# Kernel tuning notes

Measured on AMD Instinct MI355X. Metric: run time of the kernel, lower is better.

The kernel has to match this reference:

```python
import jax, jax.numpy as jnp
import numpy as np

SCALE = 32 ** (-0.5)  # hardcoded in the original module, independent of head_size

def setup_inputs() -> dict:
    key = jax.random.key(0)
    k1, k2, k3, k4 = jax.random.split(key, 4)
    B, T, E, H = 8, 4096, 2048, 128
    x = jax.random.normal(k1, (B, T, E), dtype=jnp.float32)
    Wq = jax.random.normal(k2, (E, H), dtype=jnp.float32) * (E ** -0.5)
    Wk = jax.random.normal(k3, (E, H), dtype=jnp.float32) * (E ** -0.5)
    Wv = jax.random.normal(k4, (E, H), dtype=jnp.float32) * (E ** -0.5)
    return {"x": x, "Wq": Wq, "Wk": Wk, "Wv": Wv}

def reference(x, Wq, Wk, Wv):
    # q,k,v: [B,T,H]
    q = jnp.einsum('bte,eh->bth', x, Wq)
    k = jnp.einsum('bte,eh->bth', x, Wk)
    v = jnp.einsum('bte,eh->bth', x, Wv)
    # wei: [B, T(query), T(key)]
    wei = jnp.einsum('bqh,bkh->bqk', q, k) * SCALE
    # NOTE: original uses F.softmax(wei, dim=1) -> normalize over the QUERY axis
    wei = jax.nn.softmax(wei, axis=1)
    # dropout prob is 0 in this deterministic baseline (eval mode)
    out = jnp.einsum('bqk,bkh->bqh', wei, v)
    return out
```

## Files before the change

### kernel.cpp

```cpp
#include <hip/hip_runtime.h>
#include <hip/hip_bf16.h>
#include <hip/hip_fp16.h>

#define Bn 8
#define Tn 4096
#define En 2048
#define Hn 128

typedef __attribute__((ext_vector_type(8))) short bf16x8;
typedef __attribute__((ext_vector_type(4))) float f32x4;
typedef __attribute__((ext_vector_type(4))) unsigned int u32x4;

typedef const __attribute__((address_space(1))) unsigned int* gptr_t;
typedef __attribute__((address_space(3))) unsigned int* lptr_t;

static __device__ __forceinline__ void gload16(const void* g, void* l) {
    __builtin_amdgcn_global_load_lds((gptr_t)g, (lptr_t)l, 16, 0, 0);
}

static __device__ __forceinline__ unsigned short f2bf(float f) {
    union { float f; unsigned u; } v; v.f = f;
    unsigned r = v.u + 0x7FFFu + ((v.u >> 16) & 1u);
    return (unsigned short)(r >> 16);
}
static __device__ __forceinline__ unsigned cvtpk(float lo, float hi) {
    unsigned r;
    asm volatile("v_cvt_pk_bf16_f32 %0, %1, %2" : "=v"(r) : "v"(lo), "v"(hi));
    return r;
}

#define MFMA16(a, b, c) __builtin_amdgcn_mfma_f32_16x16x32_bf16((a), (b), (c), 0, 0, 0)
#define EXP2F(x) __builtin_amdgcn_exp2f(x)
#define WAIT_VM_PUB(N) do { asm volatile("s_waitcnt vmcnt(" #N ")" ::: "memory"); \
                            __builtin_amdgcn_sched_barrier(0); \
                            __builtin_amdgcn_s_barrier(); \
                            __builtin_amdgcn_sched_barrier(0); } while (0)
#define LGKM_BARRIER() do { asm volatile("s_waitcnt lgkmcnt(0)" ::: "memory"); \
                            __builtin_amdgcn_s_barrier(); \
                            __builtin_amdgcn_sched_barrier(0); } while (0)

__global__ __launch_bounds__(256) void prep_w(const float* __restrict__ Wq,
                                              const float* __restrict__ Wk,
                                              const float* __restrict__ Wv,
                                              unsigned short* __restrict__ Wt) {
    int idx = blockIdx.x * 256 + threadIdx.x;
    int w = idx / (En * Hn);
    int rem = idx - w * (En * Hn);
    int kx = rem >> 7;
    int n  = rem & 127;
    const float* W = (w == 0) ? Wq : (w == 1) ? Wk : Wv;
    float f = W[rem];
    if (w == 0) f *= (0.17677669529663687f * 1.4426950408889634f);
    Wt[(size_t)w * En * Hn + (size_t)n * En + kx] = f2bf(f);
}

__global__ __launch_bounds__(256, 3) void qkv_mfma(const float* __restrict__ x,
                                                   const unsigned short* __restrict__ Wt,
                                                   unsigned short* __restrict__ qs,
                                                   unsigned short* __restrict__ ks,
                                                   unsigned short* __restrict__ vT) {
    __shared__ __align__(16) float Al[128][64];
    __shared__ __align__(16) unsigned short Bl[128][64];
    const int bid = blockIdx.x;
    const int w = bid % 3;
    const int m0 = (bid / 3) * 128;
    const int b = m0 >> 12;
    const int tb = m0 & (Tn - 1);
    const int t = threadIdx.x;
    const int lane = t & 63, wid = t >> 6;
    const int wr = (wid >> 1) * 64, wc = (wid & 1) * 64;
    const int fr = lane & 15, fq = lane >> 4;
    const unsigned short* Wb = Wt + (size_t)w * En * Hn;
    const int aR = lane >> 4, aC = lane & 15;
    const int bR = lane >> 3, bC = lane & 7;

    f32x4 acc[4][4] = {};
    for (int k0 = 0; k0 < En; k0 += 64) {
        __syncthreads();
        #pragma unroll
        for (int s = 0; s < 8; ++s) {
            int seg = wid * 8 + s;
            int r = seg * 4 + aR;
            gload16(&x[(size_t)(m0 + r) * En + k0 + ((aC ^ (r & 15)) * 4)],
                    (char*)Al + seg * 1024 + lane * 16);
        }
        #pragma unroll
        for (int s = 0; s < 4; ++s) {
            int seg = wid * 4 + s;
            int r = seg * 8 + bR;
            gload16(&Wb[(size_t)r * En + k0 + ((bC ^ (r & 7)) * 8)],
                    (char*)Bl + seg * 1024 + lane * 16);
        }
        __syncthreads();
        #pragma unroll
        for (int ksub = 0; ksub < 2; ++ksub) {
            bf16x8 av[4], bv[4];
            #pragma unroll
            for (int mi = 0; mi < 4; ++mi) {
                int row = wr + mi * 16 + fr;
                const char* base = (const char*)Al + row * 256;
                int c0 = ksub * 8 + fq * 2;
                f32x4 a0 = *(const f32x4*)(base + ((c0 ^ (row & 15)) << 4));
                f32x4 a1 = *(const f32x4*)(base + (((c0 + 1) ^ (row & 15)) << 4));
                u32x4 pk;
                pk[0] = cvtpk(a0[0], a0[1]);
                pk[1] = cvtpk(a0[2], a0[3]);
                pk[2] = cvtpk(a1[0], a1[1]);
                pk[3] = cvtpk(a1[2], a1[3]);
                av[mi] = *reinterpret_cast<bf16x8*>(&pk);
            }
            #pragma unroll
            for (int ni = 0; ni < 4; ++ni) {
                int row = wc + ni * 16 + fr;
                int ch = (ksub * 4 + fq) ^ (row & 7);
                bv[ni] = *reinterpret_cast<const bf16x8*>((const char*)Bl + row * 128 + ch * 16);
            }
            #pragma unroll
            for (int mi = 0; mi < 4; ++mi)
                #pragma unroll
                for (int ni = 0; ni < 4; ++ni)
                    acc[mi][ni] = MFMA16(av[mi], bv[ni], acc[mi][ni]);
        }
    }

    if (w < 2) {
        unsigned short* out = (w == 0) ? qs : ks;
        #pragma unroll
        for (int mi = 0; mi < 4; ++mi)
            #pragma unroll
            for (int ni = 0; ni < 4; ++ni)
                #pragma unroll
                for (int r = 0; r < 4; ++r) {
                    int row = m0 + wr + mi * 16 + fq * 4 + r;
                    int col = wc + ni * 16 + fr;
                    out[(size_t)row * Hn + col] = f2bf(acc[mi][ni][r]);
                }
    } else {
        #pragma unroll
        for (int mi = 0; mi < 4; ++mi)
            #pragma unroll
            for (int ni = 0; ni < 4; ++ni)
                #pragma unroll
                for (int r = 0; r < 4; ++r) {
                    int tt = tb + wr + mi * 16 + fq * 4 + r;
                    int h  = wc + ni * 16 + fr;
                    vT[((size_t)b * Hn + h) * Tn + tt] = f2bf(acc[mi][ni][r]);
                }
    }
}

__global__ __launch_bounds__(256, 3) void stats_qk(const unsigned short* __restrict__ qs,
                                                   const unsigned short* __restrict__ ks,
                                                   float2* __restrict__ part) {
    __shared__ __align__(16) char smem[49152];
    const int bid = blockIdx.x;
    const int b = bid & 7;
    const int rest = bid >> 3;
    const int kt = rest & 63;
    const int qh = rest >> 6;
    const int k0 = kt * 64;
    const unsigned short* qb = qs + (size_t)b * Tn * Hn;
    const unsigned short* kb = ks + (size_t)b * Tn * Hn;
    const int t = threadIdx.x;
    const int lane = t & 63, wid = t >> 6;
    const int wk = wid >> 1, wq = wid & 1;
    const int fr = lane & 15, fq = lane >> 4;
    const int srow = t >> 4, schk = t & 15;

    #pragma unroll
    for (int it = 0; it < 4; ++it) {
        int r = it * 16 + srow;
        gload16(&kb[(size_t)(k0 + r) * Hn + ((schk ^ (r & 15)) * 8)],
                smem + it * 4096 + t * 16);
        gload16(&qb[(size_t)(qh * 2048 + r) * Hn + ((schk ^ (r & 15)) * 8)],
                smem + 16384 + it * 4096 + t * 16);
    }
    __syncthreads();
    bf16x8 av[2][4];
    #pragma unroll
    for (int mi = 0; mi < 2; ++mi)
        #pragma unroll
        for (int kc = 0; kc < 4; ++kc) {
            int row = wk * 32 + mi * 16 + fr;
            int ch = (kc * 4 + fq) ^ (row & 15);
            av[mi][kc] = *reinterpret_cast<const bf16x8*>(smem + row * 256 + ch * 16);
        }

    float m[2][4], l[2][4];
    #pragma unroll
    for (int mi = 0; mi < 2; ++mi)
        #pragma unroll
        for (int r = 0; r < 4; ++r) { m[mi][r] = -INFINITY; l[mi][r] = 0.f; }

    for (int step = 0; step < 32; ++step) {
        const int cur = step & 1;
        const int qn = qh * 2048 + ((step + 1) & 31) * 64;
        #pragma unroll
        for (int it = 0; it < 4; ++it) {
            int r = it * 16 + srow;
            gload16(&qb[(size_t)(qn + r) * Hn + ((schk ^ (r & 15)) * 8)],
                    smem + 16384 + (cur ^ 1) * 16384 + it * 4096 + t * 16);
        }
        WAIT_VM_PUB(4);
        const char* Qc = smem + 16384 + cur * 16384;
        f32x4 acc[2][2] = {};
        __builtin_amdgcn_s_setprio(1);
        #pragma unroll
        for (int kc = 0; kc < 4; ++kc) {
            bf16x8 bv[2];
            #pragma unroll
            for (int ni = 0; ni < 2; ++ni) {
                int row = wq * 32 + ni * 16 + fr;
                int ch = (kc * 4 + fq) ^ (row & 15);
                bv[ni] = *reinterpret_cast<const bf16x8*>(Qc + row * 256 + ch * 16);
            }
            #pragma unroll
            for (int mi = 0; mi < 2; ++mi)
                #pragma unroll
                for (int ni = 0; ni < 2; ++ni)
                    acc[mi][ni] = MFMA16(av[mi][kc], bv[ni], acc[mi][ni]);
        }
        __builtin_amdgcn_s_setprio(0);
        #pragma unroll
        for (int mi = 0; mi < 2; ++mi)
            #pragma unroll
            for (int r = 0; r < 4; ++r) {
                float v0 = acc[mi][0][r], v1 = acc[mi][1][r];
                float mn = fmaxf(m[mi][r], fmaxf(v0, v1));
                l[mi][r] = l[mi][r] * EXP2F(m[mi][r] - mn) + EXP2F(v0 - mn) + EXP2F(v1 - mn);
                m[mi][r] = mn;
            }
        LGKM_BARRIER();
    }
    #pragma unroll
    for (int off = 1; off <= 8; off <<= 1) {
        #pragma unroll
        for (int mi = 0; mi < 2; ++mi)
            #pragma unroll
            for (int r = 0; r < 4; ++r) {
                float mo = __shfl_xor(m[mi][r], off);
                float lo = __shfl_xor(l[mi][r], off);
                float mn = fmaxf(m[mi][r], mo);
                l[mi][r] = l[mi][r] * EXP2F(m[mi][r] - mn) + lo * EXP2F(mo - mn);
                m[mi][r] = mn;
            }
    }
    if (fr == 0) {
        #pragma unroll
        for (int mi = 0; mi < 2; ++mi)
            #pragma unroll
            for (int r = 0; r < 4; ++r) {
                int k = k0 + wk * 32 + mi * 16 + fq * 4 + r;
                part[((size_t)b * Tn + k) * 4 + qh * 2 + wq] = make_float2(m[mi][r], l[mi][r]);
            }
    }
}

__global__ __launch_bounds__(256) void stats_comb(const float2* __restrict__ part,
                                                  float* __restrict__ mr) {
    int g = blockIdx.x * 256 + threadIdx.x;
    const float2* pp = part + (size_t)g * 4;
    float2 p0 = pp[0], p1 = pp[1], p2 = pp[2], p3 = pp[3];
    float M = fmaxf(fmaxf(p0.x, p1.x), fmaxf(p2.x, p3.x));
    float L = p0.y * EXP2F(p0.x - M) + p1.y * EXP2F(p1.x - M) +
              p2.y * EXP2F(p2.x - M) + p3.y * EXP2F(p3.x - M);
    mr[g] = M + __log2f(L);
}

__global__ __launch_bounds__(256, 2) void attn_pv(const unsigned short* __restrict__ qs,
                                                  const unsigned short* __restrict__ ks,
                                                  const unsigned short* __restrict__ vT,
                                                  const float* __restrict__ mr,
                                                  float* __restrict__ out) {
    __shared__ __align__(16) char smem[73728];
    char* Pb = smem + 65536;
    const int bid = blockIdx.x;
    const int b = bid & 7;
    const int q0 = (bid >> 3) * 64;
    const unsigned short* qg = qs + (size_t)b * Tn * Hn;
    const unsigned short* kg = ks + (size_t)b * Tn * Hn;
    const unsigned short* vg = vT + (size_t)b * Hn * Tn;
    const float* mrb = mr + (size_t)b * Tn;
    const int t = threadIdx.x;
    const int lane = t & 63, wid = t >> 6;
    const int wk = wid >> 1, wq = wid & 1;
    const int fr = lane & 15, fq = lane >> 4;
    const int srow16 = t >> 4, schk16 = t & 15;
    const int srow8 = t >> 3, schk8 = t & 7;

    bf16x8 bq[2][4];
    #pragma unroll
    for (int ni = 0; ni < 2; ++ni)
        #pragma unroll
        for (int kc = 0; kc < 4; ++kc) {
            int row = q0 + wq * 32 + ni * 16 + fr;
            bq[ni][kc] = *reinterpret_cast<const bf16x8*>(&qg[(size_t)row * Hn + kc * 32 + fq * 8]);
        }
    #pragma unroll
    for (int it = 0; it < 4; ++it) {
        int r = it * 16 + srow16;
        gload16(&kg[(size_t)r * Hn + ((schk16 ^ (r & 15)) * 8)], smem + it * 4096 + t * 16);
        int rv = it * 32 + srow8;
        gload16(&vg[(size_t)rv * Tn + ((schk8 ^ (rv & 7)) * 8)],
                smem + 32768 + it * 4096 + t * 16);
    }
    __syncthreads();

    f32x4 acc_o[4][2] = {};
    for (int kt = 0; kt < 64; ++kt) {
        const int cur = kt & 1;
        const int k0 = kt * 64;
        float4 mk0 = *reinterpret_cast<const float4*>(&mrb[k0 + wk * 32 + fq * 4]);
        float4 mk1 = *reinterpret_cast<const float4*>(&mrb[k0 + wk * 32 + 16 + fq * 4]);
        __builtin_amdgcn_sched_barrier(0);
        {
            const int knr = ((kt + 1) & 63) * 64;
            #pragma unroll
            for (int it = 0; it < 4; ++it) {
                int r = it * 16 + srow16;
                gload16(&kg[(size_t)(knr + r) * Hn + ((schk16 ^ (r & 15)) * 8)],
                        smem + (cur ^ 1) * 16384 + it * 4096 + t * 16);
                int rv = it * 32 + srow8;
                gload16(&vg[(size_t)rv * Tn + knr + ((schk8 ^ (rv & 7)) * 8)],
                        smem + 32768 + (cur ^ 1) * 16384 + it * 4096 + t * 16);
            }
        }
        WAIT_VM_PUB(8);
        const char* Kc = smem + cur * 16384;
        f32x4 acc_s[2][2] = {};
        __builtin_amdgcn_s_setprio(1);
        #pragma unroll
        for (int kc = 0; kc < 4; ++kc) {
            bf16x8 avk[2];
            #pragma unroll
            for (int mi = 0; mi < 2; ++mi) {
                int row = wk * 32 + mi * 16 + fr;
                int ch = (kc * 4 + fq) ^ (row & 15);
                avk[mi] = *reinterpret_cast<const bf16x8*>(Kc + row * 256 + ch * 16);
            }
            #pragma unroll
            for (int mi = 0; mi < 2; ++mi)
                #pragma unroll
                for (int ni = 0; ni < 2; ++ni)
                    acc_s[mi][ni] = MFMA16(avk[mi], bq[ni][kc], acc_s[mi][ni]);
        }
        __builtin_amdgcn_s_setprio(0);
        #pragma unroll
        for (int mi = 0; mi < 2; ++mi) {
            float4 mk = mi ? mk1 : mk0;
            #pragma unroll
            for (int ni = 0; ni < 2; ++ni) {
                float e0 = EXP2F(acc_s[mi][ni][0] - mk.x);
                float e1 = EXP2F(acc_s[mi][ni][1] - mk.y);
                float e2 = EXP2F(acc_s[mi][ni][2] - mk.z);
                float e3 = EXP2F(acc_s[mi][ni][3] - mk.w);
                int q = wq * 32 + ni * 16 + fr;
                int chunk = (wk * 4 + mi * 2 + (fq >> 1)) ^ (q & 7);
                *reinterpret_cast<uint2*>(Pb + q * 128 + chunk * 16 + (fq & 1) * 8) =
                    make_uint2(cvtpk(e0, e1), cvtpk(e2, e3));
            }
        }
        LGKM_BARRIER();
        const char* Vc = smem + 32768 + cur * 16384;
        __builtin_amdgcn_s_setprio(1);
        #pragma unroll
        for (int kc = 0; kc < 2; ++kc) {
            bf16x8 bp[2];
            #pragma unroll
            for (int ni = 0; ni < 2; ++ni) {
                int qrow = wq * 32 + ni * 16 + fr;
                int ch = (kc * 4 + fq) ^ (qrow & 7);
                bp[ni] = *reinterpret_cast<const bf16x8*>(Pb + qrow * 128 + ch * 16);
            }
            #pragma unroll
            for (int mi = 0; mi < 4; ++mi) {
                int row = wk * 64 + mi * 16 + fr;
                int ch = (kc * 4 + fq) ^ (row & 7);
                bf16x8 avv = *reinterpret_cast<const bf16x8*>(Vc + row * 128 + ch * 16);
                #pragma unroll
                for (int ni = 0; ni < 2; ++ni)
                    acc_o[mi][ni] = MFMA16(avv, bp[ni], acc_o[mi][ni]);
            }
        }
        __builtin_amdgcn_s_setprio(0);
        LGKM_BARRIER();
    }

    float* Ol = (float*)smem;
    __syncthreads();
    #pragma unroll
    for (int mi = 0; mi < 4; ++mi)
        #pragma unroll
        for (int ni = 0; ni < 2; ++ni) {
            int q = wq * 32 + ni * 16 + fr;
            int h = wk * 64 + mi * 16 + fq * 4;
            *reinterpret_cast<float4*>(&Ol[q * 132 + h]) =
                make_float4(acc_o[mi][ni][0], acc_o[mi][ni][1], acc_o[mi][ni][2], acc_o[mi][ni][3]);
        }
    __syncthreads();
    #pragma unroll
    for (int j = 0; j < 8; ++j) {
        int idx = j * 256 + t;
        int row = idx >> 5, c = (idx & 31) * 4;
        *reinterpret_cast<float4*>(&out[((size_t)b * Tn + q0 + row) * Hn + c]) =
            *reinterpret_cast<const float4*>(&Ol[row * 132 + c]);
    }
}

extern "C" void kernel_launch(void* const* d_in, const int* in_sizes, int n_in,
                              void* d_out, int out_size, void* d_ws, size_t ws_size,
                              hipStream_t stream) {
    const float* x  = (const float*)d_in[0];
    const float* Wq = (const float*)d_in[1];
    const float* Wk = (const float*)d_in[2];
    const float* Wv = (const float*)d_in[3];
    float* out = (float*)d_out;

    char* p = (char*)d_ws;
    unsigned short* qs = (unsigned short*)p; p += (size_t)Bn * Tn * Hn * 2;
    unsigned short* ks = (unsigned short*)p; p += (size_t)Bn * Tn * Hn * 2;
    unsigned short* vT = (unsigned short*)p; p += (size_t)Bn * Tn * Hn * 2;
    unsigned short* Wt = (unsigned short*)p; p += (size_t)3 * En * Hn * 2;
    float2* part       = (float2*)p;         p += (size_t)Bn * Tn * 4 * sizeof(float2);
    float* mr          = (float*)p;          p += (size_t)Bn * Tn * sizeof(float);
    size_t needed = (size_t)(p - (char*)d_ws);
    if (ws_size < needed) return;

    prep_w<<<dim3(3 * En * Hn / 256), dim3(256), 0, stream>>>(Wq, Wk, Wv, Wt);
    qkv_mfma<<<dim3((Bn * Tn / 128) * 3), dim3(256), 0, stream>>>(x, Wt, qs, ks, vT);
    stats_qk<<<dim3(Bn * 64 * 2), dim3(256), 0, stream>>>(qs, ks, part);
    stats_comb<<<dim3(Bn * Tn / 256), dim3(256), 0, stream>>>(part, mr);
    attn_pv<<<dim3(Bn * 64), dim3(256), 0, stream>>>(qs, ks, vT, mr, out);
}
```

Before: 276.2 us.

## Fold softmax normalizer into V, split keys in attn_pv, enlarge stats_qk tiles

Adds a scale_v kernel that multiplies V by exp2(-mr[k]) per key, so attn_pv only needs exp2(s) with no per-key max subtraction. attn_pv is restructured to split the key range into two halves per block and process two query tiles per block, reusing each K/V tile across both. Partial outputs go to a workspace and a new combine kernel sums them. stats_qk now uses 128-key tiles so each streamed Q tile feeds more MFMA work, at lower occupancy. The cost is extra memory traffic for vn, the fp32 partial outputs and the combine pass, plus exposure to exp2 range without max subtraction.

```diff
diff --git a/kernel.cpp b/kernel.cpp
--- a/kernel.cpp
+++ b/kernel.cpp
@@ -22,6 +22,10 @@
     union { float f; unsigned u; } v; v.f = f;
     unsigned r = v.u + 0x7FFFu + ((v.u >> 16) & 1u);
     return (unsigned short)(r >> 16);
+}
+static __device__ __forceinline__ float b2f(unsigned short bits) {
+    union { unsigned u; float f; } v; v.u = ((unsigned)bits) << 16;
+    return v.f;
 }
 static __device__ __forceinline__ unsigned cvtpk(float lo, float hi) {
     unsigned r;
@@ -149,16 +153,16 @@
     }
 }
 
-__global__ __launch_bounds__(256, 3) void stats_qk(const unsigned short* __restrict__ qs,
+__global__ __launch_bounds__(256, 2) void stats_qk(const unsigned short* __restrict__ qs,
                                                    const unsigned short* __restrict__ ks,
                                                    float2* __restrict__ part) {
-    __shared__ __align__(16) char smem[49152];
+    __shared__ __align__(16) char smem[65536];
     const int bid = blockIdx.x;
     const int b = bid & 7;
     const int rest = bid >> 3;
-    const int kt = rest & 63;
-    const int qh = rest >> 6;
-    const int k0 = kt * 64;
+    const int kt = rest & 31;
+    const int qh = rest >> 5;
+    const int k0 = kt * 128;
     const unsigned short* qb = qs + (size_t)b * Tn * Hn;
     const unsigned short* kb = ks + (size_t)b * Tn * Hn;
     const int t = threadIdx.x;
@@ -168,27 +172,31 @@
     const int srow = t >> 4, schk = t & 15;
 
     #pragma unroll
-    for (int it = 0; it < 4; ++it) {
+    for (int it = 0; it < 8; ++it) {
         int r = it * 16 + srow;
         gload16(&kb[(size_t)(k0 + r) * Hn + ((schk ^ (r & 15)) * 8)],
                 smem + it * 4096 + t * 16);
+    }
+    #pragma unroll
+    for (int it = 0; it < 4; ++it) {
+        int r = it * 16 + srow;
         gload16(&qb[(size_t)(qh * 2048 + r) * Hn + ((schk ^ (r & 15)) * 8)],
-                smem + 16384 + it * 4096 + t * 16);
+                smem + 32768 + it * 4096 + t * 16);
     }
     __syncthreads();
-    bf16x8 av[2][4];
-    #pragma unroll
-    for (int mi = 0; mi < 2; ++mi)
+    bf16x8 av[4][4];
+    #pragma unroll
+    for (int mi = 0; mi < 4; ++mi)
         #pragma unroll
         for (int kc = 0; kc < 4; ++kc) {
-            int row = wk * 32 + mi * 16 + fr;
+            int row = wk * 64 + mi * 16 + fr;
             int ch = (kc * 4 + fq) ^ (row & 15);
             av[mi][kc] = *reinterpret_cast<const bf16x8*>(smem + row * 256 + ch * 16);
         }
 
-    float m[2][4], l[2][4];
-    #pragma unroll
-    for (int mi = 0; mi < 2; ++mi)
+    float m[4][4], l[4][4];
+    #pragma unroll
+    for (int mi = 0; mi < 4; ++mi)
         #pragma unroll
         for (int r = 0; r < 4; ++r) { m[mi][r] = -INFINITY; l[mi][r] = 0.f; }
 
@@ -199,11 +207,11 @@
         for (int it = 0; it < 4; ++it) {
             int r = it * 16 + srow;
             gload16(&qb[(size_t)(qn + r) * Hn + ((schk ^ (r & 15)) * 8)],
-                    smem + 16384 + (cur ^ 1) * 16384 + it * 4096 + t * 16);
+                    smem + 32768 + (cur ^ 1) * 16384 + it * 4096 + t * 16);
         }
         WAIT_VM_PUB(4);
-        const char* Qc = smem + 16384 + cur * 16384;
-        f32x4 acc[2][2] = {};
+        const char* Qc = smem + 32768 + cur * 16384;
+        f32x4 acc[4][2] = {};
         __builtin_amdgcn_s_setprio(1);
         #pragma unroll
         for (int kc = 0; kc < 4; ++kc) {
@@ -215,14 +223,14 @@
                 bv[ni] = *reinterpret_cast<const bf16x8*>(Qc + row * 256 + ch * 16);
             }
             #pragma unroll
-            for (int mi = 0; mi < 2; ++mi)
+            for (int mi = 0; mi < 4; ++mi)
                 #pragma unroll
                 for (int ni = 0; ni < 2; ++ni)
                     acc[mi][ni] = MFMA16(av[mi][kc], bv[ni], acc[mi][ni]);
         }
         __builtin_amdgcn_s_setprio(0);
         #pragma unroll
-        for (int mi = 0; mi < 2; ++mi)
+        for (int mi = 0; mi < 4; ++mi)
             #pragma unroll
             for (int r = 0; r < 4; ++r) {
                 float v0 = acc[mi][0][r], v1 = acc[mi][1][r];
@@ -235,7 +243,7 @@
     #pragma unroll
     for (int off = 1; off <= 8; off <<= 1) {
         #pragma unroll
-        for (int mi = 0; mi < 2; ++mi)
+        for (int mi = 0; mi < 4; ++mi)
             #pragma unroll
             for (int r = 0; r < 4; ++r) {
                 float mo = __shfl_xor(m[mi][r], off);
@@ -247,10 +255,10 @@
     }
     if (fr == 0) {
         #pragma unroll
-        for (int mi = 0; mi < 2; ++mi)
+        for (int mi = 0; mi < 4; ++mi)
             #pragma unroll
             for (int r = 0; r < 4; ++r) {
-                int k = k0 + wk * 32 + mi * 16 + fq * 4 + r;
+                int k = k0 + wk * 64 + mi * 16 + fq * 4 + r;
                 part[((size_t)b * Tn + k) * 4 + qh * 2 + wq] = make_float2(m[mi][r], l[mi][r]);
             }
     }
@@ -267,20 +275,39 @@
     mr[g] = M + __log2f(L);
 }
 
+__global__ __launch_bounds__(256) void scale_v(const unsigned short* __restrict__ vT,
+                                               const float* __restrict__ mr,
+                                               unsigned short* __restrict__ vn) {
+    size_t i = ((size_t)blockIdx.x * 256 + threadIdx.x) * 8;
+    int t0 = (int)(i & (Tn - 1));
+    int b = (int)(i >> 19);
+    const float* mrb = mr + (size_t)b * Tn + t0;
+    ushort4 v0 = *reinterpret_cast<const ushort4*>(vT + i);
+    ushort4 v1 = *reinterpret_cast<const ushort4*>(vT + i + 4);
+    float4 s0 = *reinterpret_cast<const float4*>(mrb);
+    float4 s1 = *reinterpret_cast<const float4*>(mrb + 4);
+    unsigned o[4];
+    o[0] = cvtpk(b2f(v0.x) * EXP2F(-s0.x), b2f(v0.y) * EXP2F(-s0.y));
+    o[1] = cvtpk(b2f(v0.z) * EXP2F(-s0.z), b2f(v0.w) * EXP2F(-s0.w));
+    o[2] = cvtpk(b2f(v1.x) * EXP2F(-s1.x), b2f(v1.y) * EXP2F(-s1.y));
+    o[3] = cvtpk(b2f(v1.z) * EXP2F(-s1.z), b2f(v1.w) * EXP2F(-s1.w));
+    *reinterpret_cast<u32x4*>(vn + i) = *reinterpret_cast<u32x4*>(o);
+}
+
 __global__ __launch_bounds__(256, 2) void attn_pv(const unsigned short* __restrict__ qs,
                                                   const unsigned short* __restrict__ ks,
-                                                  const unsigned short* __restrict__ vT,
-                                                  const float* __restrict__ mr,
-                                                  float* __restrict__ out) {
-    __shared__ __align__(16) char smem[73728];
-    char* Pb = smem + 65536;
+                                                  const unsigned short* __restrict__ vn,
+                                                  float* __restrict__ opart) {
+    __shared__ __align__(16) char smem[81920];
     const int bid = blockIdx.x;
     const int b = bid & 7;
-    const int q0 = (bid >> 3) * 64;
+    const int rest = bid >> 3;
+    const int qp = rest & 31;
+    const int kh = rest >> 5;
+    const int kbase = kh * 2048;
     const unsigned short* qg = qs + (size_t)b * Tn * Hn;
     const unsigned short* kg = ks + (size_t)b * Tn * Hn;
-    const unsigned short* vg = vT + (size_t)b * Hn * Tn;
-    const float* mrb = mr + (size_t)b * Tn;
+    const unsigned short* vg = vn + (size_t)b * Hn * Tn;
     const int t = threadIdx.x;
     const int lane = t & 63, wid = t >> 6;
     const int wk = wid >> 1, wq = wid & 1;
@@ -288,33 +315,35 @@
     const int srow16 = t >> 4, schk16 = t & 15;
     const int srow8 = t >> 3, schk8 = t & 7;
 
-    bf16x8 bq[2][4];
-    #pragma unroll
-    for (int ni = 0; ni < 2; ++ni)
-        #pragma unroll
-        for (int kc = 0; kc < 4; ++kc) {
-            int row = q0 + wq * 32 + ni * 16 + fr;
-            bq[ni][kc] = *reinterpret_cast<const bf16x8*>(&qg[(size_t)row * Hn + kc * 32 + fq * 8]);
-        }
+    bf16x8 bq[2][2][4];
+    #pragma unroll
+    for (int qt = 0; qt < 2; ++qt) {
+        int qb0 = qp * 64 + qt * 2048;
+        #pragma unroll
+        for (int ni = 0; ni < 2; ++ni)
+            #pragma unroll
+            for (int kc = 0; kc < 4; ++kc) {
+                int row = qb0 + wq * 32 + ni * 16 + fr;
+                bq[qt][ni][kc] = *reinterpret_cast<const bf16x8*>(
+                    &qg[(size_t)row * Hn + kc * 32 + fq * 8]);
+            }
+    }
     #pragma unroll
     for (int it = 0; it < 4; ++it) {
         int r = it * 16 + srow16;
-        gload16(&kg[(size_t)r * Hn + ((schk16 ^ (r & 15)) * 8)], smem + it * 4096 + t * 16);
+        gload16(&kg[(size_t)(kbase + r) * Hn + ((schk16 ^ (r & 15)) * 8)],
+                smem + it * 4096 + t * 16);
         int rv = it * 32 + srow8;
-        gload16(&vg[(size_t)rv * Tn + ((schk8 ^ (rv & 7)) * 8)],
+        gload16(&vg[(size_t)rv * Tn + kbase + ((schk8 ^ (rv & 7)) * 8)],
                 smem + 32768 + it * 4096 + t * 16);
     }
     __syncthreads();
 
-    f32x4 acc_o[4][2] = {};
-    for (int kt = 0; kt < 64; ++kt) {
-        const int cur = kt & 1;
-        const int k0 = kt * 64;
-        float4 mk0 = *reinterpret_cast<const float4*>(&mrb[k0 + wk * 32 + fq * 4]);
-        float4 mk1 = *reinterpret_cast<const float4*>(&mrb[k0 + wk * 32 + 16 + fq * 4]);
-        __builtin_amdgcn_sched_barrier(0);
+    f32x4 acc_o[2][4][2] = {};
+    for (int s = 0; s < 32; ++s) {
+        const int cur = s & 1;
         {
-            const int knr = ((kt + 1) & 63) * 64;
+            const int knr = kbase + ((s + 1) & 31) * 64;
             #pragma unroll
             for (int it = 0; it < 4; ++it) {
                 int r = it * 16 + srow16;
@@ -327,59 +356,66 @@
         }
         WAIT_VM_PUB(8);
         const char* Kc = smem + cur * 16384;
-        f32x4 acc_s[2][2] = {};
-        __builtin_amdgcn_s_setprio(1);
-        #pragma unroll
-        for (int kc = 0; kc < 4; ++kc) {
-            bf16x8 avk[2];
-            #pragma unroll
-            for (int mi = 0; mi < 2; ++mi) {
-                int row = wk * 32 + mi * 16 + fr;
-                int ch = (kc * 4 + fq) ^ (row & 15);
-                avk[mi] = *reinterpret_cast<const bf16x8*>(Kc + row * 256 + ch * 16);
-            }
+        #pragma unroll
+        for (int qt = 0; qt < 2; ++qt) {
+            char* Pb = smem + 65536 + qt * 8192;
+            f32x4 acc_s[2][2] = {};
+            __builtin_amdgcn_s_setprio(1);
+            #pragma unroll
+            for (int kc = 0; kc < 4; ++kc) {
+                bf16x8 avk[2];
+                #pragma unroll
+                for (int mi = 0; mi < 2; ++mi) {
+                    int row = wk * 32 + mi * 16 + fr;
+                    int ch = (kc * 4 + fq) ^ (row & 15);
+                    avk[mi] = *reinterpret_cast<const bf16x8*>(Kc + row * 256 + ch * 16);
+                }
+                #pragma unroll
+                for (int mi = 0; mi < 2; ++mi)
+                    #pragma unroll
+                    for (int ni = 0; ni < 2; ++ni)
+                        acc_s[mi][ni] = MFMA16(avk[mi], bq[qt][ni][kc], acc_s[mi][ni]);
+            }
+            __builtin_amdgcn_s_setprio(0);
             #pragma unroll
             for (int mi = 0; mi < 2; ++mi)
                 #pragma unroll
-                for (int ni = 0; ni < 2; ++ni)
-                    acc_s[mi][ni] = MFMA16(avk[mi], bq[ni][kc], acc_s[mi][ni]);
-        }
-        __builtin_amdgcn_s_setprio(0);
-        #pragma unroll
-        for (int mi = 0; mi < 2; ++mi) {
-            float4 mk = mi ? mk1 : mk0;
-            #pragma unroll
-            for (int ni = 0; ni < 2; ++ni) {
-                float e0 = EXP2F(acc_s[mi][ni][0] - mk.x);
-                float e1 = EXP2F(acc_s[mi][ni][1] - mk.y);
-                float e2 = EXP2F(acc_s[mi][ni][2] - mk.z);
-                float e3 = EXP2F(acc_s[mi][ni][3] - mk.w);
-                int q = wq * 32 + ni * 16 + fr;
-                int chunk = (wk * 4 + mi * 2 + (fq >> 1)) ^ (q & 7);
-                *reinterpret_cast<uint2*>(Pb + q * 128 + chunk * 16 + (fq & 1) * 8) =
-                    make_uint2(cvtpk(e0, e1), cvtpk(e2, e3));
-            }
+                for (int ni = 0; ni < 2; ++ni) {
+                    float e0 = EXP2F(acc_s[mi][ni][0]);
+                    float e1 = EXP2F(acc_s[mi][ni][1]);
+                    float e2 = EXP2F(acc_s[mi][ni][2]);
+                    float e3 = EXP2F(acc_s[mi][ni][3]);
+                    int q = wq * 32 + ni * 16 + fr;
+                    int chunk = (wk * 4 + mi * 2 + (fq >> 1)) ^ (q & 7);
+                    *reinterpret_cast<uint2*>(Pb + q * 128 + chunk * 16 + (fq & 1) * 8) =
+                        make_uint2(cvtpk(e0, e1), cvtpk(e2, e3));
+                }
         }
         LGKM_BARRIER();
         const char* Vc = smem + 32768 + cur * 16384;
         __builtin_amdgcn_s_setprio(1);
         #pragma unroll
         for (int kc = 0; kc < 2; ++kc) {
-            bf16x8 bp[2];
-            #pragma unroll
-            for (int ni = 0; ni < 2; ++ni) {
-                int qrow = wq * 32 + ni * 16 + fr;
-                int ch = (kc * 4 + fq) ^ (qrow & 7);
-                bp[ni] = *reinterpret_cast<const bf16x8*>(Pb + qrow * 128 + ch * 16);
-            }
+            bf16x8 bp[2][2];
+            #pragma unroll
+            for (int qt = 0; qt < 2; ++qt)
+                #pragma unroll
+                for (int ni = 0; ni < 2; ++ni) {
+                    int qrow = wq * 32 + ni * 16 + fr;
+                    int ch = (kc * 4 + fq) ^ (qrow & 7);
+                    bp[qt][ni] = *reinterpret_cast<const bf16x8*>(
+                        smem + 65536 + qt * 8192 + qrow * 128 + ch * 16);
+                }
             #pragma unroll
             for (int mi = 0; mi < 4; ++mi) {
                 int row = wk * 64 + mi * 16 + fr;
                 int ch = (kc * 4 + fq) ^ (row & 7);
                 bf16x8 avv = *reinterpret_cast<const bf16x8*>(Vc + row * 128 + ch * 16);
                 #pragma unroll
-                for (int ni = 0; ni < 2; ++ni)
-                    acc_o[mi][ni] = MFMA16(avv, bp[ni], acc_o[mi][ni]);
+                for (int qt = 0; qt < 2; ++qt)
+                    #pragma unroll
+                    for (int ni = 0; ni < 2; ++ni)
+                        acc_o[qt][mi][ni] = MFMA16(avv, bp[qt][ni], acc_o[qt][mi][ni]);
             }
         }
         __builtin_amdgcn_s_setprio(0);
@@ -388,23 +424,40 @@
 
     float* Ol = (float*)smem;
     __syncthreads();
-    #pragma unroll
-    for (int mi = 0; mi < 4; ++mi)
-        #pragma unroll
-        for (int ni = 0; ni < 2; ++ni) {
-            int q = wq * 32 + ni * 16 + fr;
-            int h = wk * 64 + mi * 16 + fq * 4;
-            *reinterpret_cast<float4*>(&Ol[q * 132 + h]) =
-                make_float4(acc_o[mi][ni][0], acc_o[mi][ni][1], acc_o[mi][ni][2], acc_o[mi][ni][3]);
-        }
-    __syncthreads();
-    #pragma unroll
-    for (int j = 0; j < 8; ++j) {
-        int idx = j * 256 + t;
-        int row = idx >> 5, c = (idx & 31) * 4;
-        *reinterpret_cast<float4*>(&out[((size_t)b * Tn + q0 + row) * Hn + c]) =
-            *reinterpret_cast<const float4*>(&Ol[row * 132 + c]);
-    }
+    float* op = opart + (size_t)kh * Bn * Tn * Hn + (size_t)b * Tn * Hn;
+    #pragma unroll
+    for (int qt = 0; qt < 2; ++qt) {
+        #pragma unroll
+        for (int mi = 0; mi < 4; ++mi)
+            #pragma unroll
+            for (int ni = 0; ni < 2; ++ni) {
+                int q = wq * 32 + ni * 16 + fr;
+                int h = wk * 64 + mi * 16 + fq * 4;
+                *reinterpret_cast<float4*>(&Ol[q * 132 + h]) =
+                    make_float4(acc_o[qt][mi][ni][0], acc_o[qt][mi][ni][1],
+                                acc_o[qt][mi][ni][2], acc_o[qt][mi][ni][3]);
+            }
+        __syncthreads();
+        int qrow0 = qp * 64 + qt * 2048;
+        #pragma unroll
+        for (int j = 0; j < 8; ++j) {
+            int idx = j * 256 + t;
+            int row = idx >> 5, c = (idx & 31) * 4;
+            *reinterpret_cast<float4*>(&op[(size_t)(qrow0 + row) * Hn + c]) =
+                *reinterpret_cast<const float4*>(&Ol[row * 132 + c]);
+        }
+        __syncthreads();
+    }
+}
+
+__global__ __launch_bounds__(256) void combine(const float* __restrict__ opart,
+                                               float* __restrict__ out) {
+    size_t i = ((size_t)blockIdx.x * 256 + threadIdx.x) * 4;
+    const size_t half = (size_t)Bn * Tn * Hn;
+    float4 a = *reinterpret_cast<const float4*>(opart + i);
+    float4 b = *reinterpret_cast<const float4*>(opart + half + i);
+    *reinterpret_cast<float4*>(out + i) =
+        make_float4(a.x + b.x, a.y + b.y, a.z + b.z, a.w + b.w);
 }
 
 extern "C" void kernel_launch(void* const* d_in, const int* in_sizes, int n_in,
@@ -420,15 +473,19 @@
     unsigned short* qs = (unsigned short*)p; p += (size_t)Bn * Tn * Hn * 2;
     unsigned short* ks = (unsigned short*)p; p += (size_t)Bn * Tn * Hn * 2;
     unsigned short* vT = (unsigned short*)p; p += (size_t)Bn * Tn * Hn * 2;
+    unsigned short* vn = (unsigned short*)p; p += (size_t)Bn * Tn * Hn * 2;
     unsigned short* Wt = (unsigned short*)p; p += (size_t)3 * En * Hn * 2;
     float2* part       = (float2*)p;         p += (size_t)Bn * Tn * 4 * sizeof(float2);
     float* mr          = (float*)p;          p += (size_t)Bn * Tn * sizeof(float);
+    float* opart       = (float*)p;          p += (size_t)2 * Bn * Tn * Hn * sizeof(float);
     size_t needed = (size_t)(p - (char*)d_ws);
     if (ws_size < needed) return;
 
     prep_w<<<dim3(3 * En * Hn / 256), dim3(256), 0, stream>>>(Wq, Wk, Wv, Wt);
     qkv_mfma<<<dim3((Bn * Tn / 128) * 3), dim3(256), 0, stream>>>(x, Wt, qs, ks, vT);
-    stats_qk<<<dim3(Bn * 64 * 2), dim3(256), 0, stream>>>(qs, ks, part);
+    stats_qk<<<dim3(512), dim3(256), 0, stream>>>(qs, ks, part);
     stats_comb<<<dim3(Bn * Tn / 256), dim3(256), 0, stream>>>(part, mr);
-    attn_pv<<<dim3(Bn * 64), dim3(256), 0, stream>>>(qs, ks, vT, mr, out);
-}
+    scale_v<<<dim3((size_t)Bn * Hn * Tn / (256 * 8)), dim3(256), 0, stream>>>(vT, mr, vn);
+    attn_pv<<<dim3(512), dim3(256), 0, stream>>>(qs, ks, vn, opart);
+    combine<<<dim3((size_t)Bn * Tn * Hn / (256 * 4)), dim3(256), 0, stream>>>(opart, out);
+}
```

New measurement: 276.1 us. No clear change (-0.0%).
